# Performance work log

Measured on AMD Instinct MI355X. Metric: run time of the kernel, lower is better.

## Reference

```python
import jax, jax.numpy as jnp
import numpy as np

B, F, V, D, A, ND = 4096, 26, 100000, 16, 16, 13


def setup_inputs() -> dict:
    key = jax.random.key(0)
    ks = jax.random.split(key, 10)
    dense_input = jax.random.normal(ks[0], (B, ND), dtype=jnp.float32)
    sparse_input = jax.random.randint(ks[1], (B, F), 0, V, dtype=jnp.int32)
    # all fields share feat_num=V, so stack tables into one [F, V, D] array
    embed_tables = jax.random.normal(ks[2], (F, V, D), dtype=jnp.float32) * 0.001
    att_W = jax.random.normal(ks[3], (D, A), dtype=jnp.float32) * (2.0 / (D + A)) ** 0.5
    att_b = jnp.zeros((A,), dtype=jnp.float32)
    att_h = jax.random.normal(ks[4], (A, 1), dtype=jnp.float32) * (2.0 / (A + 1)) ** 0.5
    att_p = jax.random.normal(ks[5], (D, 1), dtype=jnp.float32) * (2.0 / (D + 1)) ** 0.5
    lin_w_dense = jax.random.normal(ks[6], (ND, 1), dtype=jnp.float32) * 0.01
    lin_w_sparse = jax.random.normal(ks[7], (F * D, 1), dtype=jnp.float32) * 0.01
    lin_b = jnp.zeros((1,), dtype=jnp.float32)
    return {"dense_input": dense_input, "sparse_input": sparse_input,
            "embed_tables": embed_tables, "att_W": att_W, "att_b": att_b,
            "att_h": att_h, "att_p": att_p, "lin_w_dense": lin_w_dense,
            "lin_w_sparse": lin_w_sparse, "lin_b": lin_b}


def reference(dense_input, sparse_input, embed_tables, att_W, att_b, att_h,
              att_p, lin_w_dense, lin_w_sparse, lin_b):
    # per-field embedding gather: [B, F, D]
    emb = embed_tables[jnp.arange(F)[None, :], sparse_input]
    sparse_concat = emb.reshape(B, F * D)
    # linear part (Linear(dense, sparse_concat) -> [B, 1])
    linear_result = dense_input @ lin_w_dense + sparse_concat @ lin_w_sparse + lin_b
    # pairwise element-wise products for i < j: [B, P, D], P = F*(F-1)/2
    iu, ju = np.triu_indices(F, k=1)
    ewp = emb[:, iu, :] * emb[:, ju, :]
    # attention MLP over pairs
    att_wx_b = jax.nn.relu(jnp.einsum('bpd,da->bpa', ewp, att_W) + att_b)
    score = jax.nn.softmax(jnp.einsum('bpa,ao->bpo', att_wx_b, att_h), axis=1)  # [B,P,1]
    att_output = jnp.sum(score * ewp, axis=1)  # [B, D]; dropout_rate=0 -> identity
    afm_result = att_output @ att_p  # [B, 1]
    return jax.nn.sigmoid(afm_result + linear_result)
```

## Files before the change

### kernel.cpp

```cpp
#include <hip/hip_runtime.h>
#include <hip/hip_bf16.h>

typedef float v2f    __attribute__((ext_vector_type(2)));
typedef float v4f    __attribute__((ext_vector_type(4)));
typedef float f32x16 __attribute__((ext_vector_type(16)));
typedef __bf16 bf16x8 __attribute__((ext_vector_type(8)));

#define BATCH 4096
#define NF 26
#define NV 100000
#define ND_ 16
#define NA 16
#define NDENSE 13
#define NPAIR 325
#define ROWP 20
#define WPB 4
#define BLOCK (WPB * 64)
#define NTILE 11

__global__ __launch_bounds__(BLOCK) void afm_kernel(
    const float* __restrict__ dense,
    const int*   __restrict__ sparse,
    const float* __restrict__ tables,
    const float* __restrict__ attW,
    const float* __restrict__ attB,
    const float* __restrict__ attH,
    const float* __restrict__ attP,
    const float* __restrict__ wDense,
    const float* __restrict__ wSparse,
    const float* __restrict__ linB,
    float* __restrict__ out)
{
    __shared__ int sOFF[NPAIR];
    __shared__ __align__(16) float sEmb[WPB][NF * ROWP];

    const int tid  = threadIdx.x;
    const int wave = tid >> 6;
    const int lane = tid & 63;
    const int col  = lane & 31;
    const int hi   = lane >> 5;
    const int b    = blockIdx.x * WPB + wave;

    int idxreg = 0;
    if (lane < NF) idxreg = sparse[b * NF + lane];

    #pragma unroll
    for (int rnd = 0; rnd < 2; ++rnd) {
        const int c = lane + rnd * 64;
        if (c < (NF * ND_) / 4) {
            const int f  = c >> 2;
            const int d4 = (c & 3) << 2;
            const int row = __shfl(idxreg, f);
            const float4 v = *reinterpret_cast<const float4*>(
                tables + ((size_t)f * NV + (size_t)row) * ND_ + d4);
            *reinterpret_cast<float4*>(&sEmb[wave][f * ROWP + d4]) = v;
        }
    }

    for (int p = tid; p < NPAIR; p += BLOCK) {
        int i = 0, rem = p;
        while (rem >= NF - 1 - i) { rem -= NF - 1 - i; ++i; }
        const int j = i + 1 + rem;
        sOFF[p] = (i * ROWP) | ((j * ROWP) << 16);
    }

    bf16x8 afrag;
    #pragma unroll
    for (int t = 0; t < 8; ++t) {
        float a = 0.f;
        if (col < NA)       a = attW[(hi * 8 + t) * NA + col];
        else if (col == NA) a = attP[hi * 8 + t];
        afrag[t] = (__bf16)a;
    }
    float  hreg[8];
    f32x16 cinit = {0.f,0.f,0.f,0.f,0.f,0.f,0.f,0.f,0.f,0.f,0.f,0.f,0.f,0.f,0.f,0.f};
    #pragma unroll
    for (int r = 0; r < 8; ++r) {
        const int k = (r & 3) + 8 * (r >> 2) + 4 * hi;
        hreg[r]  = attH[k];
        cinit[r] = attB[k];
    }

    __syncthreads();

    const float* __restrict__ semb = sEmb[wave];

    float lin = 0.f;
    #pragma unroll
    for (int rnd = 0; rnd < 7; ++rnd) {
        const int e = lane + rnd * 64;
        if (e < NF * ND_)
            lin += semb[(e >> 4) * ROWP + (e & 15)] * wSparse[e];
    }
    if (lane < NDENSE)
        lin += dense[b * NDENSE + lane] * wDense[lane];

    float num = 0.f, den = 0.f;
    #pragma unroll
    for (int t = 0; t < NTILE; ++t) {
        const int p     = t * 32 + col;
        const bool valid = (p < NPAIR) && (hi == 0);
        const int pc    = (p < NPAIR) ? p : (NPAIR - 1);
        const int offs  = sOFF[pc];
        const float* ri = semb + (offs & 0xffff) + hi * 8;
        const float* rj = semb + (offs >> 16)    + hi * 8;

        const v4f x0 = *reinterpret_cast<const v4f*>(ri);
        const v4f x1 = *reinterpret_cast<const v4f*>(ri + 4);
        const v4f y0 = *reinterpret_cast<const v4f*>(rj);
        const v4f y1 = *reinterpret_cast<const v4f*>(rj + 4);
        const v4f e0 = x0 * y0;
        const v4f e1 = x1 * y1;

        bf16x8 bfrag;
        bfrag[0] = (__bf16)e0[0]; bfrag[1] = (__bf16)e0[1];
        bfrag[2] = (__bf16)e0[2]; bfrag[3] = (__bf16)e0[3];
        bfrag[4] = (__bf16)e1[0]; bfrag[5] = (__bf16)e1[1];
        bfrag[6] = (__bf16)e1[2]; bfrag[7] = (__bf16)e1[3];

        const f32x16 acc =
            __builtin_amdgcn_mfma_f32_32x32x16_bf16(afrag, bfrag, cinit, 0, 0, 0);

        v2f sp2 = {0.f, 0.f};
        #pragma unroll
        for (int r = 0; r < 4; ++r) {
            v2f z;  z.x = acc[2 * r];  z.y = acc[2 * r + 1];
            v2f zr; zr.x = fmaxf(z.x, 0.f); zr.y = fmaxf(z.y, 0.f);
            v2f h;  h.x = hreg[2 * r]; h.y = hreg[2 * r + 1];
            sp2 = zr * h + sp2;
        }
        const float sp = sp2.x + sp2.y;
        const float sfull = sp + __shfl_xor(sp, 32);

        const float ev = valid ? __expf(sfull) : 0.f;
        num = fmaf(ev, acc[8], num);
        den += ev;
    }

    #pragma unroll
    for (int o = 32; o; o >>= 1) {
        num += __shfl_xor(num, o);
        den += __shfl_xor(den, o);
        lin += __shfl_xor(lin, o);
    }
    if (lane == 0) {
        const float x = num / den + lin + linB[0];
        out[b] = 1.f / (1.f + __expf(-x));
    }
}

extern "C" void kernel_launch(void* const* d_in, const int* in_sizes, int n_in,
                              void* d_out, int out_size, void* d_ws, size_t ws_size,
                              hipStream_t stream) {
    const float* dense   = (const float*)d_in[0];
    const int*   sparse  = (const int*)d_in[1];
    const float* tables  = (const float*)d_in[2];
    const float* attW    = (const float*)d_in[3];
    const float* attB    = (const float*)d_in[4];
    const float* attH    = (const float*)d_in[5];
    const float* attP    = (const float*)d_in[6];
    const float* wDense  = (const float*)d_in[7];
    const float* wSparse = (const float*)d_in[8];
    const float* linB    = (const float*)d_in[9];
    float* out = (float*)d_out;

    const int grid = BATCH / WPB;
    afm_kernel<<<grid, BLOCK, 0, stream>>>(
        dense, sparse, tables, attW, attB, attH, attP,
        wDense, wSparse, linB, out);
}
```

Measured before the change: 14.87 us.

## Store gathered embeddings as bf16 in LDS and fuse linear term into gather

Embeddings are converted to bf16 when written to shared memory, so each pair tile loads two 16-byte vectors instead of four. Products are computed from the unpacked bf16 values. The sparse linear dot product moves into the gather loop, reading wSparse as float4 and dropping a separate pass over LDS. The cost is lower precision in the pairwise products, since inputs are rounded to bf16 before multiplying, and some extra unpacking ALU work.

```diff
diff --git a/kernel.cpp b/kernel.cpp
--- a/kernel.cpp
+++ b/kernel.cpp
@@ -13,10 +13,17 @@
 #define NA 16
 #define NDENSE 13
 #define NPAIR 325
-#define ROWP 20
+#define ROWB 24
 #define WPB 4
 #define BLOCK (WPB * 64)
 #define NTILE 11
+
+static __device__ __forceinline__ float bflo(unsigned int u) {
+    return __builtin_bit_cast(float, u << 16);
+}
+static __device__ __forceinline__ float bfhi(unsigned int u) {
+    return __builtin_bit_cast(float, u & 0xffff0000u);
+}
 
 __global__ __launch_bounds__(BLOCK) void afm_kernel(
     const float* __restrict__ dense,
@@ -32,7 +39,7 @@
     float* __restrict__ out)
 {
     __shared__ int sOFF[NPAIR];
-    __shared__ __align__(16) float sEmb[WPB][NF * ROWP];
+    __shared__ __align__(16) unsigned short sEmbB[WPB][NF * ROWB];
 
     const int tid  = threadIdx.x;
     const int wave = tid >> 6;
@@ -44,6 +51,7 @@
     int idxreg = 0;
     if (lane < NF) idxreg = sparse[b * NF + lane];
 
+    float lin = 0.f;
     #pragma unroll
     for (int rnd = 0; rnd < 2; ++rnd) {
         const int c = lane + rnd * 64;
@@ -53,15 +61,24 @@
             const int row = __shfl(idxreg, f);
             const float4 v = *reinterpret_cast<const float4*>(
                 tables + ((size_t)f * NV + (size_t)row) * ND_ + d4);
-            *reinterpret_cast<float4*>(&sEmb[wave][f * ROWP + d4]) = v;
+            const float4 w = *reinterpret_cast<const float4*>(wSparse + f * ND_ + d4);
+            lin += v.x * w.x + v.y * w.y + v.z * w.z + v.w * w.w;
+            ushort4 pk;
+            pk.x = __builtin_bit_cast(unsigned short, (__bf16)v.x);
+            pk.y = __builtin_bit_cast(unsigned short, (__bf16)v.y);
+            pk.z = __builtin_bit_cast(unsigned short, (__bf16)v.z);
+            pk.w = __builtin_bit_cast(unsigned short, (__bf16)v.w);
+            *reinterpret_cast<ushort4*>(&sEmbB[wave][f * ROWB + d4]) = pk;
         }
     }
+    if (lane < NDENSE)
+        lin += dense[b * NDENSE + lane] * wDense[lane];
 
     for (int p = tid; p < NPAIR; p += BLOCK) {
         int i = 0, rem = p;
         while (rem >= NF - 1 - i) { rem -= NF - 1 - i; ++i; }
         const int j = i + 1 + rem;
-        sOFF[p] = (i * ROWP) | ((j * ROWP) << 16);
+        sOFF[p] = (i * ROWB) | ((j * ROWB) << 16);
     }
 
     bf16x8 afrag;
@@ -83,17 +100,7 @@
 
     __syncthreads();
 
-    const float* __restrict__ semb = sEmb[wave];
-
-    float lin = 0.f;
-    #pragma unroll
-    for (int rnd = 0; rnd < 7; ++rnd) {
-        const int e = lane + rnd * 64;
-        if (e < NF * ND_)
-            lin += semb[(e >> 4) * ROWP + (e & 15)] * wSparse[e];
-    }
-    if (lane < NDENSE)
-        lin += dense[b * NDENSE + lane] * wDense[lane];
+    const unsigned short* __restrict__ base = sEmbB[wave];
 
     float num = 0.f, den = 0.f;
     #pragma unroll
@@ -102,21 +109,19 @@
         const bool valid = (p < NPAIR) && (hi == 0);
         const int pc    = (p < NPAIR) ? p : (NPAIR - 1);
         const int offs  = sOFF[pc];
-        const float* ri = semb + (offs & 0xffff) + hi * 8;
-        const float* rj = semb + (offs >> 16)    + hi * 8;
 
-        const v4f x0 = *reinterpret_cast<const v4f*>(ri);
-        const v4f x1 = *reinterpret_cast<const v4f*>(ri + 4);
-        const v4f y0 = *reinterpret_cast<const v4f*>(rj);
-        const v4f y1 = *reinterpret_cast<const v4f*>(rj + 4);
-        const v4f e0 = x0 * y0;
-        const v4f e1 = x1 * y1;
+        const uint4 ui = *reinterpret_cast<const uint4*>(base + (offs & 0xffff) + hi * 8);
+        const uint4 uj = *reinterpret_cast<const uint4*>(base + (offs >> 16)    + hi * 8);
 
         bf16x8 bfrag;
-        bfrag[0] = (__bf16)e0[0]; bfrag[1] = (__bf16)e0[1];
-        bfrag[2] = (__bf16)e0[2]; bfrag[3] = (__bf16)e0[3];
-        bfrag[4] = (__bf16)e1[0]; bfrag[5] = (__bf16)e1[1];
-        bfrag[6] = (__bf16)e1[2]; bfrag[7] = (__bf16)e1[3];
+        bfrag[0] = (__bf16)(bflo(ui.x) * bflo(uj.x));
+        bfrag[1] = (__bf16)(bfhi(ui.x) * bfhi(uj.x));
+        bfrag[2] = (__bf16)(bflo(ui.y) * bflo(uj.y));
+        bfrag[3] = (__bf16)(bfhi(ui.y) * bfhi(uj.y));
+        bfrag[4] = (__bf16)(bflo(ui.z) * bflo(uj.z));
+        bfrag[5] = (__bf16)(bfhi(ui.z) * bfhi(uj.z));
+        bfrag[6] = (__bf16)(bflo(ui.w) * bflo(uj.w));
+        bfrag[7] = (__bf16)(bfhi(ui.w) * bfhi(uj.w));
 
         const f32x16 acc =
             __builtin_amdgcn_mfma_f32_32x32x16_bf16(afrag, bfrag, cinit, 0, 0, 0);
```

After: 15.84 us. 6.5% more time.

## Split each batch item across two waves and combine partial softmax sums

Applied to the files above, without the earlier changes.

Each batch item is now handled by two waves instead of one, with 512-thread blocks still covering four items. The gather, linear-term and MFMA pair-tile loops are split between the two waves, and the partial num/den/lin values are combined through shared memory after an extra barrier. The attention bias is now added after the MFMA instead of being used as the accumulator init. This halves the serial per-wave work to raise parallelism and shorten latency per item, at the cost of an extra __syncthreads and more waves per block.

```diff
diff --git a/kernel.cpp b/kernel.cpp
--- a/kernel.cpp
+++ b/kernel.cpp
@@ -15,10 +15,10 @@
 #define NPAIR 325
 #define ROWP 20
 #define WPB 4
-#define BLOCK (WPB * 64)
+#define BLOCK 512
 #define NTILE 11
 
-__global__ __launch_bounds__(BLOCK) void afm_kernel(
+__global__ __launch_bounds__(BLOCK, 8) void afm_kernel(
     const float* __restrict__ dense,
     const int*   __restrict__ sparse,
     const float* __restrict__ tables,
@@ -33,35 +33,37 @@
 {
     __shared__ int sOFF[NPAIR];
     __shared__ __align__(16) float sEmb[WPB][NF * ROWP];
+    __shared__ float sPart[WPB][2][3];
 
     const int tid  = threadIdx.x;
     const int wave = tid >> 6;
     const int lane = tid & 63;
+    const int item = wave >> 1;
+    const int subw = wave & 1;
     const int col  = lane & 31;
     const int hi   = lane >> 5;
-    const int b    = blockIdx.x * WPB + wave;
+    const int b    = blockIdx.x * WPB + item;
 
     int idxreg = 0;
     if (lane < NF) idxreg = sparse[b * NF + lane];
 
-    #pragma unroll
-    for (int rnd = 0; rnd < 2; ++rnd) {
-        const int c = lane + rnd * 64;
+    {
+        const int c = subw * 64 + lane;
         if (c < (NF * ND_) / 4) {
             const int f  = c >> 2;
             const int d4 = (c & 3) << 2;
             const int row = __shfl(idxreg, f);
             const float4 v = *reinterpret_cast<const float4*>(
                 tables + ((size_t)f * NV + (size_t)row) * ND_ + d4);
-            *reinterpret_cast<float4*>(&sEmb[wave][f * ROWP + d4]) = v;
+            *reinterpret_cast<float4*>(&sEmb[item][f * ROWP + d4]) = v;
         }
     }
 
-    for (int p = tid; p < NPAIR; p += BLOCK) {
-        int i = 0, rem = p;
+    if (tid < NPAIR) {
+        int i = 0, rem = tid;
         while (rem >= NF - 1 - i) { rem -= NF - 1 - i; ++i; }
         const int j = i + 1 + rem;
-        sOFF[p] = (i * ROWP) | ((j * ROWP) << 16);
+        sOFF[tid] = (i * ROWP) | ((j * ROWP) << 16);
     }
 
     bf16x8 afrag;
@@ -72,70 +74,74 @@
         else if (col == NA) a = attP[hi * 8 + t];
         afrag[t] = (__bf16)a;
     }
-    float  hreg[8];
-    f32x16 cinit = {0.f,0.f,0.f,0.f,0.f,0.f,0.f,0.f,0.f,0.f,0.f,0.f,0.f,0.f,0.f,0.f};
+    v2f h2[4], b2[4];
     #pragma unroll
     for (int r = 0; r < 8; ++r) {
         const int k = (r & 3) + 8 * (r >> 2) + 4 * hi;
-        hreg[r]  = attH[k];
-        cinit[r] = attB[k];
+        h2[r >> 1][r & 1] = attH[k];
+        b2[r >> 1][r & 1] = attB[k];
     }
 
     __syncthreads();
 
-    const float* __restrict__ semb = sEmb[wave];
+    const float* __restrict__ semb = sEmb[item];
 
     float lin = 0.f;
     #pragma unroll
-    for (int rnd = 0; rnd < 7; ++rnd) {
-        const int e = lane + rnd * 64;
+    for (int rnd = 0; rnd < 4; ++rnd) {
+        const int e = subw * 64 + lane + rnd * 128;
         if (e < NF * ND_)
             lin += semb[(e >> 4) * ROWP + (e & 15)] * wSparse[e];
     }
-    if (lane < NDENSE)
+    if (subw == 0 && lane < NDENSE)
         lin += dense[b * NDENSE + lane] * wDense[lane];
 
     float num = 0.f, den = 0.f;
-    #pragma unroll
-    for (int t = 0; t < NTILE; ++t) {
-        const int p     = t * 32 + col;
-        const bool valid = (p < NPAIR) && (hi == 0);
-        const int pc    = (p < NPAIR) ? p : (NPAIR - 1);
-        const int offs  = sOFF[pc];
-        const float* ri = semb + (offs & 0xffff) + hi * 8;
-        const float* rj = semb + (offs >> 16)    + hi * 8;
+    auto tiles = [&](const int t0, const int NT) {
+        #pragma unroll
+        for (int tt = 0; tt < NT; ++tt) {
+            const int t     = t0 + tt;
+            const int p     = t * 32 + col;
+            const bool valid = (p < NPAIR) && (hi == 0);
+            const int pc    = (p < NPAIR) ? p : (NPAIR - 1);
+            const int offs  = sOFF[pc];
+            const float* ri = semb + (offs & 0xffff) + hi * 8;
+            const float* rj = semb + (offs >> 16)    + hi * 8;
 
-        const v4f x0 = *reinterpret_cast<const v4f*>(ri);
-        const v4f x1 = *reinterpret_cast<const v4f*>(ri + 4);
-        const v4f y0 = *reinterpret_cast<const v4f*>(rj);
-        const v4f y1 = *reinterpret_cast<const v4f*>(rj + 4);
-        const v4f e0 = x0 * y0;
-        const v4f e1 = x1 * y1;
+            const v4f x0 = *reinterpret_cast<const v4f*>(ri);
+            const v4f x1 = *reinterpret_cast<const v4f*>(ri + 4);
+            const v4f y0 = *reinterpret_cast<const v4f*>(rj);
+            const v4f y1 = *reinterpret_cast<const v4f*>(rj + 4);
+            const v4f e0 = x0 * y0;
+            const v4f e1 = x1 * y1;
 
-        bf16x8 bfrag;
-        bfrag[0] = (__bf16)e0[0]; bfrag[1] = (__bf16)e0[1];
-        bfrag[2] = (__bf16)e0[2]; bfrag[3] = (__bf16)e0[3];
-        bfrag[4] = (__bf16)e1[0]; bfrag[5] = (__bf16)e1[1];
-        bfrag[6] = (__bf16)e1[2]; bfrag[7] = (__bf16)e1[3];
+            bf16x8 bfrag;
+            bfrag[0] = (__bf16)e0[0]; bfrag[1] = (__bf16)e0[1];
+            bfrag[2] = (__bf16)e0[2]; bfrag[3] = (__bf16)e0[3];
+            bfrag[4] = (__bf16)e1[0]; bfrag[5] = (__bf16)e1[1];
+            bfrag[6] = (__bf16)e1[2]; bfrag[7] = (__bf16)e1[3];
 
-        const f32x16 acc =
-            __builtin_amdgcn_mfma_f32_32x32x16_bf16(afrag, bfrag, cinit, 0, 0, 0);
+            f32x16 acc = {0.f,0.f,0.f,0.f,0.f,0.f,0.f,0.f,
+                          0.f,0.f,0.f,0.f,0.f,0.f,0.f,0.f};
+            acc = __builtin_amdgcn_mfma_f32_32x32x16_bf16(afrag, bfrag, acc, 0, 0, 0);
 
-        v2f sp2 = {0.f, 0.f};
-        #pragma unroll
-        for (int r = 0; r < 4; ++r) {
-            v2f z;  z.x = acc[2 * r];  z.y = acc[2 * r + 1];
-            v2f zr; zr.x = fmaxf(z.x, 0.f); zr.y = fmaxf(z.y, 0.f);
-            v2f h;  h.x = hreg[2 * r]; h.y = hreg[2 * r + 1];
-            sp2 = zr * h + sp2;
+            v2f sp2 = {0.f, 0.f};
+            #pragma unroll
+            for (int r = 0; r < 4; ++r) {
+                v2f z; z.x = acc[2 * r]; z.y = acc[2 * r + 1];
+                z = z + b2[r];
+                v2f zr; zr.x = fmaxf(z.x, 0.f); zr.y = fmaxf(z.y, 0.f);
+                sp2 = zr * h2[r] + sp2;
+            }
+            const float sp = sp2.x + sp2.y;
+            const float sfull = sp + __shfl_xor(sp, 32);
+
+            const float ev = valid ? __expf(sfull) : 0.f;
+            num = fmaf(ev, acc[8], num);
+            den += ev;
         }
-        const float sp = sp2.x + sp2.y;
-        const float sfull = sp + __shfl_xor(sp, 32);
-
-        const float ev = valid ? __expf(sfull) : 0.f;
-        num = fmaf(ev, acc[8], num);
-        den += ev;
-    }
+    };
+    if (subw == 0) tiles(0, 6); else tiles(6, 5);
 
     #pragma unroll
     for (int o = 32; o; o >>= 1) {
@@ -144,7 +150,17 @@
         lin += __shfl_xor(lin, o);
     }
     if (lane == 0) {
-        const float x = num / den + lin + linB[0];
+        sPart[item][subw][0] = num;
+        sPart[item][subw][1] = den;
+        sPart[item][subw][2] = lin;
+    }
+    __syncthreads();
+
+    if (subw == 0 && lane == 0) {
+        const float n = sPart[item][0][0] + sPart[item][1][0];
+        const float d = sPart[item][0][1] + sPart[item][1][1];
+        const float l = sPart[item][0][2] + sPart[item][1][2];
+        const float x = n / d + l + linB[0];
         out[b] = 1.f / (1.f + __expf(-x));
     }
 }
```

Result: faster. 14.09 us (-5.2%).
